# Kernel tuning notes

Measured on AMD Instinct MI355X. Metric: run time of the kernel, lower is better.

The kernel has to match this reference:

```python
import jax, jax.numpy as jnp
import numpy as np

B, C, NX, NY = 4, 64, 432, 496
G = NX * NY
P_PER = 20000


def setup_inputs() -> dict:
    key = jax.random.key(0)
    ks = jax.random.split(key, 4)
    rng = np.random.default_rng(0)
    coords = []
    for b in range(B):
        flat = rng.choice(G, P_PER, replace=False)  # unique BEV cells per batch
        y, x = flat // NX, flat % NX
        coords.append(np.stack([np.full(P_PER, b), np.zeros(P_PER, np.int64), y, x], 1))
    coords = jnp.asarray(np.concatenate(coords, 0), dtype=jnp.int32)  # [P,4] = (b,z,y,x)
    return {
        "pillar_features": jax.random.normal(ks[0], (B * P_PER, C), jnp.float32),
        "W_off": jax.random.normal(ks[1], (2, C), jnp.float32) * 0.05,
        "b_off": jnp.zeros((2,), jnp.float32),
        "W_step": jax.random.normal(ks[2], (1, C), jnp.float32) * 0.05,
        "b_step": jnp.zeros((1,), jnp.float32),
        "W_prob": jax.random.normal(ks[3], (1, C), jnp.float32) * 0.05,
        "b_prob": jnp.zeros((1,), jnp.float32),
        "voxel_coords": coords,
    }


def reference(pillar_features, W_off, b_off, W_step, b_step, W_prob, b_prob, voxel_coords):
    # flat scatter index per pillar: batch*G + (z + y*nx + x), nz==1 so z==0
    b_idx = voxel_coords[:, 0].astype(jnp.int32)
    idx = voxel_coords[:, 1] + voxel_coords[:, 2] * NX + voxel_coords[:, 3]
    gidx = b_idx * G + idx  # [P]

    # dense BEV scatter (indices are unique per batch -> set semantics match torch)
    spatial = jnp.zeros((B * G, C), pillar_features.dtype).at[gidx].set(pillar_features)

    # VotingModule heads on pillar features
    offset = jnp.tanh(pillar_features @ W_off.T + b_off)          # [P,2]
    step = jax.nn.relu(pillar_features @ W_step.T + b_step)       # [P,1]
    prob = jax.nn.sigmoid(pillar_features @ W_prob.T + b_prob)    # [P,1]

    cent = jnp.zeros((B * G, 2), pillar_features.dtype).at[gidx].set(offset)
    # NOTE: original code writes step then immediately overwrites with prob (bug kept)
    step_buf = jnp.zeros((B * G, 1), pillar_features.dtype).at[gidx].set(prob)
    prob_buf = jnp.zeros((B * G, 1), pillar_features.dtype)  # never written (bug kept)

    # get_propagatated_feature: shift features by offset*step, weighted by prob
    off_y = cent[:, 0] * step_buf[:, 0]
    off_x = cent[:, 1] * step_buf[:, 0]
    yy = jnp.tile(jnp.repeat(jnp.arange(NY), NX), B).astype(jnp.float32)
    xx = jnp.tile(jnp.tile(jnp.arange(NX), NY), B).astype(jnp.float32)
    ty = jnp.clip(jnp.round(yy + off_y), 0, NY - 1).astype(jnp.int32)
    tx = jnp.clip(jnp.round(xx + off_x), 0, NX - 1).astype(jnp.int32)
    bb = jnp.repeat(jnp.arange(B, dtype=jnp.int32), G)
    tgt = bb * G + ty * NX + tx  # [B*G]

    p = prob_buf  # [B*G,1]
    out = jnp.zeros((B * G, C), spatial.dtype).at[tgt].add(spatial * p) + spatial * (1.0 - p)
    return out.reshape(B, NY, NX, C).transpose(0, 3, 1, 2)  # [B,C,ny,nx]
```

## Files before the change

### kernel.cpp

```cpp
#include <hip/hip_runtime.h>
#include <hip/hip_bf16.h>

#define BB 4
#define CC 64
#define NXX 432
#define NYY 496
#define GG (NXX * NYY)
#define PP 80000


__global__ void k_init_map(int* __restrict__ map) {
    int i = blockIdx.x * blockDim.x + threadIdx.x;
    const int n4 = (BB * GG) / 4;
    if (i < n4) {
        ((int4*)map)[i] = make_int4(-1, -1, -1, -1);
    }
}

__global__ void k_scatter_ids(const int* __restrict__ coords, int* __restrict__ map) {
    int i = blockIdx.x * blockDim.x + threadIdx.x;
    if (i < PP) {
        int4 cd = ((const int4*)coords)[i];
        int g = cd.x * GG + cd.y + cd.z * NXX + cd.w;
        map[g] = i;
    }
}

__global__ void k_gather(const float* __restrict__ pf,
                         const int* __restrict__ map,
                         float* __restrict__ out) {
    int t = blockIdx.x * blockDim.x + threadIdx.x;
    const int nGroups = (BB * GG) / 4;
    if (t >= nGroups) return;

    int cellBase = t * 4;
    int b = cellBase / GG;
    int cellInB = cellBase - b * GG;

    int4 pids = ((const int4*)map)[t];
    const float4* pf4 = (const float4*)pf;
    const float4 zero = make_float4(0.f, 0.f, 0.f, 0.f);

    float* outBase = out + (size_t)(b * CC) * GG + cellInB;

    int c0base = blockIdx.y * 16;

    #pragma unroll
    for (int cg = 0; cg < 4; ++cg) {
        int c0 = c0base + cg * 4;
        int q = c0 >> 2;
        float4 r0 = (pids.x >= 0) ? pf4[pids.x * 16 + q] : zero;
        float4 r1 = (pids.y >= 0) ? pf4[pids.y * 16 + q] : zero;
        float4 r2 = (pids.z >= 0) ? pf4[pids.z * 16 + q] : zero;
        float4 r3 = (pids.w >= 0) ? pf4[pids.w * 16 + q] : zero;

        float4 w0 = make_float4(r0.x, r1.x, r2.x, r3.x);
        float4 w1 = make_float4(r0.y, r1.y, r2.y, r3.y);
        float4 w2 = make_float4(r0.z, r1.z, r2.z, r3.z);
        float4 w3 = make_float4(r0.w, r1.w, r2.w, r3.w);

        *((float4*)(outBase + (size_t)(c0 + 0) * GG)) = w0;
        *((float4*)(outBase + (size_t)(c0 + 1) * GG)) = w1;
        *((float4*)(outBase + (size_t)(c0 + 2) * GG)) = w2;
        *((float4*)(outBase + (size_t)(c0 + 3) * GG)) = w3;
    }
}

extern "C" void kernel_launch(void* const* d_in, const int* in_sizes, int n_in,
                              void* d_out, int out_size, void* d_ws, size_t ws_size,
                              hipStream_t stream) {
    const float* pf     = (const float*)d_in[0];
    const int*   coords = (const int*)d_in[7];
    float*       out    = (float*)d_out;
    int*         map    = (int*)d_ws;

    const int n4 = (BB * GG) / 4;
    k_init_map<<<dim3((n4 + 255) / 256), dim3(256), 0, stream>>>(map);
    k_scatter_ids<<<dim3((PP + 255) / 256), dim3(256), 0, stream>>>(coords, map);

    const int nGroups = (BB * GG) / 4;
    dim3 grid((nGroups + 255) / 256, 4);
    k_gather<<<grid, dim3(256), 0, stream>>>(pf, map, out);
}
```

Baseline: 252.9 us.

## Use nontemporal stores, unconditional loads, and one thread for all channels

```diff
diff --git a/kernel.cpp b/kernel.cpp
--- a/kernel.cpp
+++ b/kernel.cpp
@@ -7,6 +7,8 @@
 #define NYY 496
 #define GG (NXX * NYY)
 #define PP 80000
+
+typedef float v4f __attribute__((ext_vector_type(4)));
 
 
 __global__ void k_init_map(int* __restrict__ map) {
@@ -38,31 +40,33 @@
     int cellInB = cellBase - b * GG;
 
     int4 pids = ((const int4*)map)[t];
-    const float4* pf4 = (const float4*)pf;
-    const float4 zero = make_float4(0.f, 0.f, 0.f, 0.f);
+    const v4f* pf4 = (const v4f*)pf;
 
+    bool v0 = pids.x >= 0, v1 = pids.y >= 0, v2 = pids.z >= 0, v3 = pids.w >= 0;
+    int i0 = (v0 ? pids.x : 0) * 16;
+    int i1 = (v1 ? pids.y : 0) * 16;
+    int i2 = (v2 ? pids.z : 0) * 16;
+    int i3 = (v3 ? pids.w : 0) * 16;
+
+    const v4f zero = (v4f)(0.f);
     float* outBase = out + (size_t)(b * CC) * GG + cellInB;
 
-    int c0base = blockIdx.y * 16;
+    #pragma unroll
+    for (int cg = 0; cg < 16; ++cg) {
+        v4f r0 = pf4[i0 + cg]; r0 = v0 ? r0 : zero;
+        v4f r1 = pf4[i1 + cg]; r1 = v1 ? r1 : zero;
+        v4f r2 = pf4[i2 + cg]; r2 = v2 ? r2 : zero;
+        v4f r3 = pf4[i3 + cg]; r3 = v3 ? r3 : zero;
 
-    #pragma unroll
-    for (int cg = 0; cg < 4; ++cg) {
-        int c0 = c0base + cg * 4;
-        int q = c0 >> 2;
-        float4 r0 = (pids.x >= 0) ? pf4[pids.x * 16 + q] : zero;
-        float4 r1 = (pids.y >= 0) ? pf4[pids.y * 16 + q] : zero;
-        float4 r2 = (pids.z >= 0) ? pf4[pids.z * 16 + q] : zero;
-        float4 r3 = (pids.w >= 0) ? pf4[pids.w * 16 + q] : zero;
+        v4f w0 = (v4f){r0.x, r1.x, r2.x, r3.x};
+        v4f w1 = (v4f){r0.y, r1.y, r2.y, r3.y};
+        v4f w2 = (v4f){r0.z, r1.z, r2.z, r3.z};
+        v4f w3 = (v4f){r0.w, r1.w, r2.w, r3.w};
 
-        float4 w0 = make_float4(r0.x, r1.x, r2.x, r3.x);
-        float4 w1 = make_float4(r0.y, r1.y, r2.y, r3.y);
-        float4 w2 = make_float4(r0.z, r1.z, r2.z, r3.z);
-        float4 w3 = make_float4(r0.w, r1.w, r2.w, r3.w);
-
-        *((float4*)(outBase + (size_t)(c0 + 0) * GG)) = w0;
-        *((float4*)(outBase + (size_t)(c0 + 1) * GG)) = w1;
-        *((float4*)(outBase + (size_t)(c0 + 2) * GG)) = w2;
-        *((float4*)(outBase + (size_t)(c0 + 3) * GG)) = w3;
+        __builtin_nontemporal_store(w0, (v4f*)(outBase + (size_t)(4 * cg + 0) * GG));
+        __builtin_nontemporal_store(w1, (v4f*)(outBase + (size_t)(4 * cg + 1) * GG));
+        __builtin_nontemporal_store(w2, (v4f*)(outBase + (size_t)(4 * cg + 2) * GG));
+        __builtin_nontemporal_store(w3, (v4f*)(outBase + (size_t)(4 * cg + 3) * GG));
     }
 }
 
@@ -79,6 +83,5 @@
     k_scatter_ids<<<dim3((PP + 255) / 256), dim3(256), 0, stream>>>(coords, map);
 
     const int nGroups = (BB * GG) / 4;
-    dim3 grid((nGroups + 255) / 256, 4);
-    k_gather<<<grid, dim3(256), 0, stream>>>(pf, map, out);
+    k_gather<<<dim3((nGroups + 255) / 256), dim3(256), 0, stream>>>(pf, map, out);
 }
```

Result: no change. 256.6 us (+1.5%).
